# Kernel tuning notes

Hardware: AMD Instinct MI355X
Metric: run time of the kernel (lower is better)

## Reference

```python
import jax, jax.numpy as jnp
import numpy as np

N, C, K, P, Q, PS = 32, 128, 128, 64, 64, 3

def setup_inputs() -> dict:
    key = jax.random.key(0)
    k1, k2, k3 = jax.random.split(key, 3)
    x = jax.random.normal(k1, (N, C, P, Q), dtype=jnp.float32)
    W = jax.random.normal(k2, (K, C * PS * PS), dtype=jnp.float32) * (1.0 / np.sqrt(C * PS * PS))
    perturbs = jax.random.normal(k3, (N, K, P, Q), dtype=jnp.float32)
    return {"x": x, "W": W, "perturbs": perturbs}

def reference(x, W, perturbs):
    # patchify (pad=1, unfold 3x3, stride 1) + matmul with W^T is exactly a
    # 3x3 SAME convolution: flatten order of patchify is (C, kh, kw), matching
    # conv.weight.reshape(k, -1). Express it as a direct conv (no im2col blowup).
    k = W.shape[0]
    c = x.shape[1]
    w = W.reshape(k, c, PS, PS)  # OIHW
    out = jax.lax.conv_general_dilated(
        x, w,
        window_strides=(1, 1),
        padding=((1, 1), (1, 1)),
        dimension_numbers=("NCHW", "OIHW", "NCHW"),
    )
    return out + perturbs
```

## Files before the change

kernel.cpp:

```cpp
#include <hip/hip_runtime.h>
#include <hip/hip_bf16.h>

#define NN 32
#define CCH 128
#define KK 128
#define PP 64
#define QQ 64

typedef __bf16 bf16x8 __attribute__((ext_vector_type(8)));
typedef float f32x16 __attribute__((ext_vector_type(16)));
typedef float f32x4 __attribute__((ext_vector_type(4)));


__global__ __launch_bounds__(256) void prep_w(const float* __restrict__ W,
                                              __bf16* __restrict__ Wf) {
    const int id = blockIdx.x * 256 + threadIdx.x;
    const int lane = id & 63;
    const int r1   = id >> 6;
    const int kb   = r1 & 3;
    const int r2   = r1 >> 2;
    const int t    = r2 % 9;
    const int cc   = r2 / 9;

    const int k  = kb * 32 + (lane & 31);
    const int c0 = cc * 16 + (lane >> 5) * 8;

    bf16x8 o;
#pragma unroll
    for (int j = 0; j < 8; ++j)
        o[j] = (__bf16)W[(size_t)k * (CCH * 9) + (size_t)(c0 + j) * 9 + t];
    ((bf16x8*)Wf)[id] = o;
}

#define XPITCH 2112
#define XROWS  6
#define XBYTES (XROWS * XPITCH)

__global__ __launch_bounds__(256, 2) void conv_main(const float* __restrict__ x,
                                                    const __bf16* __restrict__ Wf,
                                                    const float* __restrict__ per,
                                                    float* __restrict__ out) {
    __shared__ __align__(16) char xlds[2][XBYTES];
    __shared__ __align__(16) char scr_lds[4][4096];

    const int tid  = threadIdx.x;
    const int lane = tid & 63;
    const int w    = tid >> 6;
    const int kbs  = w & 1;
    const int pb   = w >> 1;
    const int n    = blockIdx.y;
    const int p0   = blockIdx.x * 4;
    const int m    = lane & 31;
    const int half = lane >> 5;

    if (tid < 24) {
        int row = tid >> 2, part = tid & 3;
        int off = row * XPITCH + (part >> 1) * 2080 + (part & 1) * 16;
        *(f32x4*)(xlds[0] + off) = f32x4{0.f, 0.f, 0.f, 0.f};
        *(f32x4*)(xlds[1] + off) = f32x4{0.f, 0.f, 0.f, 0.f};
    }

    f32x16 acc[2][2][2];
#pragma unroll
    for (int a = 0; a < 2; ++a)
#pragma unroll
        for (int b = 0; b < 2; ++b)
#pragma unroll
            for (int c = 0; c < 2; ++c)
#pragma unroll
                for (int e = 0; e < 16; ++e) acc[a][b][c][e] = 0.f;

    const float* xn = x + (size_t)n * CCH * PP * QQ;

    auto stage = [&](int ccn, int buf) {
        const float* xs = xn + (size_t)ccn * 16 * PP * QQ;
#pragma unroll
        for (int it = 0; it < 3; ++it) {
            int t4  = it * 4 + w;
            int row = t4 >> 1;
            int ch  = t4 & 1;
            int r   = p0 - 1 + row;
            int rc  = r < 0 ? 0 : (r > 63 ? 63 : r);
            const float* src = xs + ((size_t)(ch * 8) * PP + rc) * QQ + lane;
            bf16x8 o;
#pragma unroll
            for (int j = 0; j < 8; ++j)
                o[j] = (__bf16)src[(size_t)j * PP * QQ];
            *(bf16x8*)(xlds[buf] + row * XPITCH + 32 + lane * 32 + ch * 16) = o;
        }
    };

    const bf16x8* wg = (const bf16x8*)Wf + kbs * 128 + lane;

    auto compute = [&](int buf, int cc) {
        const char* xbase = xlds[buf];
        const bf16x8* wc = wg + (size_t)cc * 2304;

        bf16x8 a_cur[3][2], a_prev[3][2];
#pragma unroll
        for (int ri = 0; ri < 4; ++ri) {
            const int rr = pb * 2 + ri;
            const int r  = p0 + pb * 2 + ri - 1;
            const bool rok = ((unsigned)r < (unsigned)PP);

            bf16x8 b[3][2];
            if (rok) {
                const char* rbase = xbase + rr * XPITCH + half * 16;
#pragma unroll
                for (int dq = 0; dq < 3; ++dq)
#pragma unroll
                    for (int qb = 0; qb < 2; ++qb)
                        b[dq][qb] = *(const bf16x8*)(rbase + (qb * 32 + m + dq) * 32);
            }

            if (ri < 3) {
#pragma unroll
                for (int dq = 0; dq < 3; ++dq)
#pragma unroll
                    for (int kb = 0; kb < 2; ++kb)
                        a_cur[dq][kb] = wc[((ri * 3 + dq) * 4 + kb) * 64];
            }

            if (rok) {
                if (ri >= 1) {
#pragma unroll
                    for (int dq = 0; dq < 3; ++dq)
#pragma unroll
                        for (int kb = 0; kb < 2; ++kb)
#pragma unroll
                            for (int qb = 0; qb < 2; ++qb)
                                acc[1][kb][qb] = __builtin_amdgcn_mfma_f32_32x32x16_bf16(
                                    a_prev[dq][kb], b[dq][qb], acc[1][kb][qb], 0, 0, 0);
                }
                if (ri < 3) {
#pragma unroll
                    for (int dq = 0; dq < 3; ++dq)
#pragma unroll
                        for (int kb = 0; kb < 2; ++kb)
#pragma unroll
                            for (int qb = 0; qb < 2; ++qb)
                                acc[0][kb][qb] = __builtin_amdgcn_mfma_f32_32x32x16_bf16(
                                    a_cur[dq][kb], b[dq][qb], acc[0][kb][qb], 0, 0, 0);
                }
            }

            if (ri < 3) {
#pragma unroll
                for (int dq = 0; dq < 3; ++dq)
#pragma unroll
                    for (int kb = 0; kb < 2; ++kb) a_prev[dq][kb] = a_cur[dq][kb];
            }
        }
    };

    stage(0, 0);
    __syncthreads();

    for (int cc = 0; cc < 7; ++cc) {
        stage(cc + 1, (cc + 1) & 1);
        compute(cc & 1, cc);
        __syncthreads();
    }

    auto tile_addr = [&](int it, int j) -> size_t {
        int oi = it >> 2, kbi = (it >> 1) & 1, qb = it & 1;
        int prow = p0 + pb * 2 + oi;
        int k = (kbs * 2 + kbi) * 32 + (lane >> 3) + j * 8;
        int q = qb * 32 + (lane & 7) * 4;
        return (((size_t)n * KK + k) * PP + prow) * QQ + q;
    };

    float* scr = (float*)scr_lds[w];

    auto process = [&](int it, f32x4 (&pv)[4]) {
        int oi = it >> 2, kbi = (it >> 1) & 1, qb = it & 1;
        f32x16 v = acc[oi][kbi][qb];
#pragma unroll
        for (int r = 0; r < 16; ++r) {
            int kl = (r & 3) + 8 * (r >> 2) + 4 * half;
            scr[kl * 32 + ((((m >> 2) ^ (kl & 7)) << 2) | (m & 3))] = v[r];
        }
#pragma unroll
        for (int j = 0; j < 4; ++j) {
            int kl = (lane >> 3) + j * 8;
            f32x4 d = *(const f32x4*)(scr + kl * 32 + (((lane & 7) ^ (kl & 7)) << 2));
            f32x4 s = d + pv[j];
            __builtin_nontemporal_store(s, (f32x4*)(out + tile_addr(it, j)));
        }
    };

    f32x4 pv0[4], pv1[4];
#pragma unroll
    for (int j = 0; j < 4; ++j) pv0[j] = *(const f32x4*)(per + tile_addr(0, j));

    compute(1, 7);

#pragma unroll
    for (int itp = 0; itp < 4; ++itp) {
        const int itA = itp * 2, itB = itp * 2 + 1;
#pragma unroll
        for (int j = 0; j < 4; ++j) pv1[j] = *(const f32x4*)(per + tile_addr(itB, j));
        process(itA, pv0);
        if (itp < 3) {
#pragma unroll
            for (int j = 0; j < 4; ++j)
                pv0[j] = *(const f32x4*)(per + tile_addr(itA + 2, j));
        }
        process(itB, pv1);
    }
}

extern "C" void kernel_launch(void* const* d_in, const int* in_sizes, int n_in,
                              void* d_out, int out_size, void* d_ws, size_t ws_size,
                              hipStream_t stream) {
    const float* x   = (const float*)d_in[0];
    const float* W   = (const float*)d_in[1];
    const float* per = (const float*)d_in[2];
    float* out = (float*)d_out;

    __bf16* Wf = (__bf16*)d_ws;

    prep_w<<<dim3(72), 256, 0, stream>>>(W, Wf);
    conv_main<<<dim3(PP / 4, NN), 256, 0, stream>>>(x, Wf, per, out);
}
```

Measured before the change: 193.1 us.

## Split x staging into register prefetch and post-compute LDS write, restructure MFMA loop

Global loads of the next channel chunk now go into registers before compute, and the bf16 conversion and LDS write happen after compute. This hides global-load latency behind the MFMA work instead of stalling on it up front. The compute loop is reorganized per output row, loading weights fresh per tap row instead of carrying a_prev/a_cur, and wraps MFMA bursts in s_setprio. Perturbation loads become nontemporal. The cost is 24 extra live float registers, which may pressure the 2-waves-per-SIMD occupancy target, plus more weight reloads from global/L2.

After: 195.1 us. Within noise of the previous version (+1.0%).

```diff
diff --git a/kernel.cpp b/kernel.cpp
--- a/kernel.cpp
+++ b/kernel.cpp
@@ -72,7 +72,7 @@
 
     const float* xn = x + (size_t)n * CCH * PP * QQ;
 
-    auto stage = [&](int ccn, int buf) {
+    auto stage_load = [&](int ccn, float (&fv)[3][8]) {
         const float* xs = xn + (size_t)ccn * 16 * PP * QQ;
 #pragma unroll
         for (int it = 0; it < 3; ++it) {
@@ -82,10 +82,19 @@
             int r   = p0 - 1 + row;
             int rc  = r < 0 ? 0 : (r > 63 ? 63 : r);
             const float* src = xs + ((size_t)(ch * 8) * PP + rc) * QQ + lane;
+#pragma unroll
+            for (int j = 0; j < 8; ++j) fv[it][j] = src[(size_t)j * PP * QQ];
+        }
+    };
+    auto stage_write = [&](int buf, const float (&fv)[3][8]) {
+#pragma unroll
+        for (int it = 0; it < 3; ++it) {
+            int t4  = it * 4 + w;
+            int row = t4 >> 1;
+            int ch  = t4 & 1;
             bf16x8 o;
 #pragma unroll
-            for (int j = 0; j < 8; ++j)
-                o[j] = (__bf16)src[(size_t)j * PP * QQ];
+            for (int j = 0; j < 8; ++j) o[j] = (__bf16)fv[it][j];
             *(bf16x8*)(xlds[buf] + row * XPITCH + 32 + lane * 32 + ch * 16) = o;
         }
     };
@@ -96,69 +105,53 @@
         const char* xbase = xlds[buf];
         const bf16x8* wc = wg + (size_t)cc * 2304;
 
-        bf16x8 a_cur[3][2], a_prev[3][2];
-#pragma unroll
-        for (int ri = 0; ri < 4; ++ri) {
-            const int rr = pb * 2 + ri;
-            const int r  = p0 + pb * 2 + ri - 1;
-            const bool rok = ((unsigned)r < (unsigned)PP);
-
-            bf16x8 b[3][2];
-            if (rok) {
-                const char* rbase = xbase + rr * XPITCH + half * 16;
-#pragma unroll
-                for (int dq = 0; dq < 3; ++dq)
-#pragma unroll
-                    for (int qb = 0; qb < 2; ++qb)
-                        b[dq][qb] = *(const bf16x8*)(rbase + (qb * 32 + m + dq) * 32);
-            }
-
-            if (ri < 3) {
-#pragma unroll
-                for (int dq = 0; dq < 3; ++dq)
-#pragma unroll
-                    for (int kb = 0; kb < 2; ++kb)
-                        a_cur[dq][kb] = wc[((ri * 3 + dq) * 4 + kb) * 64];
-            }
-
-            if (rok) {
-                if (ri >= 1) {
+#pragma unroll
+        for (int oi = 0; oi < 2; ++oi) {
+#pragma unroll
+            for (int tr = 0; tr < 3; ++tr) {
+                const int ri = oi + tr;
+                const int r  = p0 + pb * 2 + ri - 1;
+                const bool rok = ((unsigned)r < (unsigned)PP);
+                if (rok) {
+                    const char* rbase = xbase + (pb * 2 + ri) * XPITCH + half * 16;
+                    bf16x8 b[3][2], a[3][2];
 #pragma unroll
                     for (int dq = 0; dq < 3; ++dq)
 #pragma unroll
+                        for (int qb = 0; qb < 2; ++qb)
+                            b[dq][qb] = *(const bf16x8*)(rbase + (qb * 32 + m + dq) * 32);
+#pragma unroll
+                    for (int dq = 0; dq < 3; ++dq)
+#pragma unroll
                         for (int kb = 0; kb < 2; ++kb)
+                            a[dq][kb] = wc[((tr * 3 + dq) * 4 + kb) * 64];
+                    __builtin_amdgcn_s_setprio(1);
+#pragma unroll
+                    for (int dq = 0; dq < 3; ++dq)
+#pragma unroll
+                        for (int kb = 0; kb < 2; ++kb)
 #pragma unroll
                             for (int qb = 0; qb < 2; ++qb)
-                                acc[1][kb][qb] = __builtin_amdgcn_mfma_f32_32x32x16_bf16(
-                                    a_prev[dq][kb], b[dq][qb], acc[1][kb][qb], 0, 0, 0);
-                }
-                if (ri < 3) {
-#pragma unroll
-                    for (int dq = 0; dq < 3; ++dq)
-#pragma unroll
-                        for (int kb = 0; kb < 2; ++kb)
-#pragma unroll
-                            for (int qb = 0; qb < 2; ++qb)
-                                acc[0][kb][qb] = __builtin_amdgcn_mfma_f32_32x32x16_bf16(
-                                    a_cur[dq][kb], b[dq][qb], acc[0][kb][qb], 0, 0, 0);
+                                acc[oi][kb][qb] = __builtin_amdgcn_mfma_f32_32x32x16_bf16(
+                                    a[dq][kb], b[dq][qb], acc[oi][kb][qb], 0, 0, 0);
+                    __builtin_amdgcn_s_setprio(0);
                 }
             }
-
-            if (ri < 3) {
-#pragma unroll
-                for (int dq = 0; dq < 3; ++dq)
-#pragma unroll
-                    for (int kb = 0; kb < 2; ++kb) a_prev[dq][kb] = a_cur[dq][kb];
-            }
-        }
-    };
-
-    stage(0, 0);
+        }
+    };
+
+    {
+        float fv[3][8];
+        stage_load(0, fv);
+        stage_write(0, fv);
+    }
     __syncthreads();
 
     for (int cc = 0; cc < 7; ++cc) {
-        stage(cc + 1, (cc + 1) & 1);
+        float fv[3][8];
+        stage_load(cc + 1, fv);
         compute(cc & 1, cc);
+        stage_write((cc + 1) & 1, fv);
         __syncthreads();
     }
 
@@ -191,7 +184,8 @@
 
     f32x4 pv0[4], pv1[4];
 #pragma unroll
-    for (int j = 0; j < 4; ++j) pv0[j] = *(const f32x4*)(per + tile_addr(0, j));
+    for (int j = 0; j < 4; ++j)
+        pv0[j] = __builtin_nontemporal_load((const f32x4*)(per + tile_addr(0, j)));
 
     compute(1, 7);
 
@@ -199,12 +193,13 @@
     for (int itp = 0; itp < 4; ++itp) {
         const int itA = itp * 2, itB = itp * 2 + 1;
 #pragma unroll
-        for (int j = 0; j < 4; ++j) pv1[j] = *(const f32x4*)(per + tile_addr(itB, j));
+        for (int j = 0; j < 4; ++j)
+            pv1[j] = __builtin_nontemporal_load((const f32x4*)(per + tile_addr(itB, j)));
         process(itA, pv0);
         if (itp < 3) {
 #pragma unroll
             for (int j = 0; j < 4; ++j)
-                pv0[j] = *(const f32x4*)(per + tile_addr(itA + 2, j));
+                pv0[j] = __builtin_nontemporal_load((const f32x4*)(per + tile_addr(itA + 2, j)));
         }
         process(itB, pv1);
     }
```
